# Performance work log

Measured on AMD Instinct MI355X. Metric: run time of the kernel, lower is better.

Reference implementation:

```python
import jax, jax.numpy as jnp
import numpy as np

N_NODES = 50000
N_EDGES = 800000
D_IN = 128
D_OUT = 128


def setup_inputs() -> dict:
    key = jax.random.key(0)
    k1, k2, k3, k4, k5 = jax.random.split(key, 5)
    x = jax.random.normal(k1, (N_NODES, D_IN), dtype=jnp.float32)
    edge_index = jax.random.randint(k2, (2, N_EDGES), 0, N_NODES, dtype=jnp.int64)
    scale = 1.0 / np.sqrt(D_IN)
    W_rel = jax.random.normal(k3, (D_OUT, D_IN), dtype=jnp.float32) * scale
    b_rel = jax.random.normal(k4, (D_OUT,), dtype=jnp.float32) * scale
    W_root = jax.random.normal(k5, (D_OUT, D_IN), dtype=jnp.float32) * scale
    return {"x": x, "edge_index": edge_index, "W_rel": W_rel, "b_rel": b_rel, "W_root": W_root}


def reference(x, edge_index, W_rel, b_rel, W_root):
    # PyG GraphConv (aggr='add'):
    #   out_i = W_rel @ (sum_{j->i} x_j) + b_rel + W_root @ x_i
    # followed by ReLU (normalization=None, dropout=0 -> identity).
    src = edge_index[0]  # message source j
    dst = edge_index[1]  # message target i
    n = x.shape[0]
    agg = jax.ops.segment_sum(x[src], dst, num_segments=n)  # [N, D_IN]
    out = agg @ W_rel.T + b_rel + x @ W_root.T              # [N, D_OUT]
    return jax.nn.relu(out)
```

## Files before the change

### kernel.cpp

```cpp
#include <hip/hip_runtime.h>
#include <hip/hip_bf16.h>


#define N_NODES 50000
#define N_EDGES 800000
#define D 128
#define SLOTS 48
#define NB 3125
#define BCAP 384
#define BINB 196
#define NPB 32
#define KC 32
#define SROW 136

#define CVT_N  (N_NODES * (D / 2))
#define PACK_N (8 * 8 * 64 * 8)

typedef __attribute__((ext_vector_type(8))) short short8;
typedef __attribute__((ext_vector_type(4))) float floatx4;

__device__ __forceinline__ float bf2f(unsigned short u) {
    return __uint_as_float((unsigned int)u << 16);
}
__device__ __forceinline__ unsigned short f2bf(float f) {
    __hip_bfloat16 h = __float2bfloat16(f);
    return *(unsigned short*)&h;
}

__device__ __forceinline__ int wave_detect_i64(const int* __restrict__ ei) {
    int lane = threadIdx.x & 63;
    int v = ei[2 * lane + 1];
    return __ballot(v == 0) == ~0ull;
}

__global__ __launch_bounds__(256) void zero_f4_kernel(float4* __restrict__ p, int n4) {
    int i = blockIdx.x * 256 + threadIdx.x;
    if (i < n4) p[i] = make_float4(0.f, 0.f, 0.f, 0.f);
}

__global__ void detect_kernel(const int* __restrict__ ei, int* __restrict__ flag) {
    if (threadIdx.x == 0 && blockIdx.x == 0) {
        int any = 0;
        for (int i = 0; i < 64; ++i) any |= ei[2 * i + 1];
        flag[0] = (any == 0) ? 1 : 0;
    }
}

__global__ __launch_bounds__(256) void stage1_kernel(const float2* __restrict__ x2,
                                                     ushort2* __restrict__ xb2,
                                                     const float* __restrict__ Wrel,
                                                     const float* __restrict__ Wroot,
                                                     unsigned short* __restrict__ pwc,
                                                     const int* __restrict__ ei,
                                                     int* __restrict__ gcur,
                                                     unsigned* __restrict__ bmem,
                                                     int* __restrict__ ovf_cnt,
                                                     int* __restrict__ ovf) {
    __shared__ int lds_cnt[NB];
    if (blockIdx.x < BINB) {
        int t = threadIdx.x;
        int i64 = wave_detect_i64(ei);
        for (int i = t; i < NB; i += 256) lds_cnt[i] = 0;
        __syncthreads();

        unsigned rec[16];
        int rnk[16];
#pragma unroll
        for (int g = 0; g < 4; ++g) {
            int base = blockIdx.x * 4096 + g * 1024 + t * 4;
            int s0 = -1, s1 = -1, s2 = -1, s3 = -1;
            int d0 = -1, d1 = -1, d2 = -1, d3 = -1;
            if (base < N_EDGES) {
                if (i64) {
                    int4 a = *(const int4*)&ei[2 * base];
                    int4 b = *(const int4*)&ei[2 * base + 4];
                    s0 = a.x; s1 = a.z; s2 = b.x; s3 = b.z;
                    int4 c = *(const int4*)&ei[2 * N_EDGES + 2 * base];
                    int4 e = *(const int4*)&ei[2 * N_EDGES + 2 * base + 4];
                    d0 = c.x; d1 = c.z; d2 = e.x; d3 = e.z;
                } else {
                    int4 sv = *(const int4*)&ei[base];
                    int4 dv = *(const int4*)&ei[N_EDGES + base];
                    s0 = sv.x; s1 = sv.y; s2 = sv.z; s3 = sv.w;
                    d0 = dv.x; d1 = dv.y; d2 = dv.z; d3 = dv.w;
                }
            }
#define BINP(idx, ss, dd)                                                        \
            {                                                                    \
                bool ok = (unsigned)(ss) < N_NODES && (unsigned)(dd) < N_NODES;  \
                rec[idx] = ok ? (((unsigned)(dd) << 16) | (unsigned)(ss))        \
                              : 0xFFFFFFFFu;                                     \
                rnk[idx] = ok ? atomicAdd(&lds_cnt[(unsigned)(dd) >> 4], 1) : 0; \
            }
            BINP(g * 4 + 0, s0, d0)
            BINP(g * 4 + 1, s1, d1)
            BINP(g * 4 + 2, s2, d2)
            BINP(g * 4 + 3, s3, d3)
#undef BINP
        }
        __syncthreads();
        for (int i = t; i < NB; i += 256) {
            int c = lds_cnt[i];
            int b = c ? atomicAdd(&gcur[i], c) : 0;
            lds_cnt[i] = b;
        }
        __syncthreads();
#pragma unroll
        for (int idx = 0; idx < 16; ++idx) {
            unsigned r = rec[idx];
            if (r != 0xFFFFFFFFu) {
                int bk = (int)(r >> 20);
                int pos = lds_cnt[bk] + rnk[idx];
                if (pos < BCAP) {
                    bmem[(size_t)bk * BCAP + pos] = r;
                } else {
                    int o = atomicAdd(ovf_cnt, 1);
                    ovf[2 * o] = (int)(r >> 16);
                    ovf[2 * o + 1] = (int)(r & 0xFFFFu);
                }
            }
        }
    } else {
        int i = (blockIdx.x - BINB) * 256 + threadIdx.x;
        if (i < CVT_N) {
            float2 f = x2[i];
            xb2[i] = make_ushort2(f2bf(f.x), f2bf(f.y));
        } else if (i < CVT_N + PACK_N) {
            int idx  = i - CVT_N;
            int j    = idx & 7;
            int lane = (idx >> 3) & 63;
            int n0   = (idx >> 9) & 7;
            int t    = idx >> 12;
            int n = n0 * 16 + (lane & 15);
            int k = t * 32 + (lane >> 4) * 8 + j;
            float w = (k < D) ? Wrel[n * D + k] : Wroot[n * D + (k - D)];
            pwc[idx] = f2bf(w);
        }
    }
}

__global__ __launch_bounds__(256) void GraphConvLayer_55783035240593_kernel(
        const ushort2* __restrict__ xb2,
        const unsigned short* __restrict__ xb,
        const int* __restrict__ gcur,
        const unsigned* __restrict__ bmem,
        const int* __restrict__ ovf_cnt,
        const int* __restrict__ ovf,
        const unsigned short* __restrict__ pwc,
        const float* __restrict__ b_rel,
        float* __restrict__ out) {
    __shared__ unsigned short sA[16 * SROW];
    __shared__ unsigned short slotsL[16 * SLOTS];
    __shared__ int lc[16];
    int t = threadIdx.x;
    int wid = t >> 6, lane = t & 63;
    int bkt = blockIdx.x;
    int node0 = bkt * 16;

    int n = gcur[bkt];
    int tov = ovf_cnt[0];
    if (t < 16) lc[t] = 0;
    __syncthreads();

    if (n > BCAP) n = BCAP;
    for (int e = t; e < n; e += 256) {
        unsigned r = bmem[(size_t)bkt * BCAP + e];
        int dl = (int)((r >> 16) & 15);
        int p = atomicAdd(&lc[dl], 1);
        if (p < SLOTS) slotsL[dl * SLOTS + p] = (unsigned short)(r & 0xFFFFu);
    }
    __syncthreads();

    for (int pp = 0; pp < 2; ++pp) {
        int la = wid * 4 + pp * 2, lb = la + 1;
        int nodeA = node0 + la, nodeB = node0 + lb;
        int kkA = lc[la], kkB = lc[lb];
        int kA = (kkA > SLOTS) ? 0 : kkA;
        int kB = (kkB > SLOTS) ? 0 : kkB;
        int myA = (lane < kA) ? (int)slotsL[la * SLOTS + lane] : 0;
        int myB = (lane < kB) ? (int)slotsL[lb * SLOTS + lane] : 0;
        float axA = 0.f, ayA = 0.f, axB = 0.f, ayB = 0.f;
        int jmax = kA > kB ? kA : kB;
        for (int j = 0; j < jmax; j += 8) {
            bool doA = j < kA, doB = j < kB;
            ushort2 u[8], v[8];
            if (doA) {
                int s[8];
#pragma unroll
                for (int i = 0; i < 8; ++i) s[i] = __shfl(myA, j + i);
#pragma unroll
                for (int i = 0; i < 8; ++i) u[i] = xb2[(size_t)s[i] * (D / 2) + lane];
            }
            if (doB) {
                int s[8];
#pragma unroll
                for (int i = 0; i < 8; ++i) s[i] = __shfl(myB, j + i);
#pragma unroll
                for (int i = 0; i < 8; ++i) v[i] = xb2[(size_t)s[i] * (D / 2) + lane];
            }
            if (doA) {
#pragma unroll
                for (int i = 0; i < 8; ++i) {
                    float mm = (j + i < kA) ? 1.f : 0.f;
                    axA += mm * bf2f(u[i].x);
                    ayA += mm * bf2f(u[i].y);
                }
            }
            if (doB) {
#pragma unroll
                for (int i = 0; i < 8; ++i) {
                    float mm = (j + i < kB) ? 1.f : 0.f;
                    axB += mm * bf2f(v[i].x);
                    ayB += mm * bf2f(v[i].y);
                }
            }
        }
        if (kkA > SLOTS) {
            for (int e = 0; e < n; ++e) {
                unsigned r = bmem[(size_t)bkt * BCAP + e];
                if ((int)(r >> 16) == nodeA) {
                    ushort2 uu = xb2[(size_t)(r & 0xFFFFu) * (D / 2) + lane];
                    axA += bf2f(uu.x); ayA += bf2f(uu.y);
                }
            }
        }
        if (kkB > SLOTS) {
            for (int e = 0; e < n; ++e) {
                unsigned r = bmem[(size_t)bkt * BCAP + e];
                if ((int)(r >> 16) == nodeB) {
                    ushort2 uu = xb2[(size_t)(r & 0xFFFFu) * (D / 2) + lane];
                    axB += bf2f(uu.x); ayB += bf2f(uu.y);
                }
            }
        }
        if (tov > 0) {
            for (int e2 = 0; e2 < tov; ++e2) {
                int dd = ovf[2 * e2];
                if (dd == nodeA) {
                    ushort2 uu = xb2[(size_t)ovf[2 * e2 + 1] * (D / 2) + lane];
                    axA += bf2f(uu.x); ayA += bf2f(uu.y);
                } else if (dd == nodeB) {
                    ushort2 uu = xb2[(size_t)ovf[2 * e2 + 1] * (D / 2) + lane];
                    axB += bf2f(uu.x); ayB += bf2f(uu.y);
                }
            }
        }
        *(ushort2*)&sA[la * SROW + 2 * lane] = make_ushort2(f2bf(axA), f2bf(ayA));
        *(ushort2*)&sA[lb * SROW + 2 * lane] = make_ushort2(f2bf(axB), f2bf(ayB));
    }
    __syncthreads();

    int m = lane & 15, quad = lane >> 4;
    const unsigned short* arow = &sA[m * SROW + quad * 8];
    const unsigned short* xrow = xb + (size_t)(node0 + m) * D + quad * 8;

    floatx4 acc0 = (floatx4){0.f, 0.f, 0.f, 0.f};
    floatx4 acc1 = (floatx4){0.f, 0.f, 0.f, 0.f};
#pragma unroll
    for (int tt = 0; tt < 8; ++tt) {
        short8 afrag = (tt < 4) ? *(const short8*)(arow + tt * 32)
                                : *(const short8*)(xrow + (tt - 4) * 32);
        const unsigned short* bb = pwc + ((size_t)(tt * 8 + wid * 2) * 64 + lane) * 8;
        short8 b0 = *(const short8*)bb;
        short8 b1 = *(const short8*)(bb + 64 * 8);
        acc0 = __builtin_amdgcn_mfma_f32_16x16x32_bf16(afrag, b0, acc0, 0, 0, 0);
        acc1 = __builtin_amdgcn_mfma_f32_16x16x32_bf16(afrag, b1, acc1, 0, 0, 0);
    }

#pragma unroll
    for (int q = 0; q < 2; ++q) {
        floatx4 a = q ? acc1 : acc0;
        int nn = (wid * 2 + q) * 16 + m;
        float bias = b_rel[nn];
#pragma unroll
        for (int r = 0; r < 4; ++r) {
            int node = node0 + quad * 4 + r;
            out[(size_t)node * D + nn] = fmaxf(a[r] + bias, 0.f);
        }
    }
}

__global__ __launch_bounds__(256) void pack_w_kernel(const float* __restrict__ W,
                                                     float* __restrict__ pw) {
    int idx = blockIdx.x * 256 + threadIdx.x;
    if (idx >= D * D) return;
    int o = idx >> 7, k = idx & 127;
    pw[k * D + o] = W[o * D + k];
}

__global__ __launch_bounds__(256) void hist_kernel(const int* __restrict__ ei,
                                                   int* __restrict__ deg) {
    int i64 = wave_detect_i64(ei);
    int base = (blockIdx.x * 256 + threadIdx.x) * 4;
    if (base >= N_EDGES) return;
    int d0, d1, d2, d3;
    if (i64) {
        int4 a = *(const int4*)&ei[2 * N_EDGES + 2 * base];
        int4 b = *(const int4*)&ei[2 * N_EDGES + 2 * base + 4];
        d0 = a.x; d1 = a.z; d2 = b.x; d3 = b.z;
    } else {
        int4 v = *(const int4*)&ei[N_EDGES + base];
        d0 = v.x; d1 = v.y; d2 = v.z; d3 = v.w;
    }
    if ((unsigned)d0 < N_NODES) atomicAdd(&deg[d0], 1);
    if ((unsigned)d1 < N_NODES) atomicAdd(&deg[d1], 1);
    if ((unsigned)d2 < N_NODES) atomicAdd(&deg[d2], 1);
    if ((unsigned)d3 < N_NODES) atomicAdd(&deg[d3], 1);
}

__device__ __forceinline__ int wave_iscan(int v, int lane) {
#pragma unroll
    for (int off = 1; off < 64; off <<= 1) {
        int u = __shfl_up(v, off, 64);
        if (lane >= off) v += u;
    }
    return v;
}

__global__ __launch_bounds__(1024) void scan_kernel(const int* __restrict__ deg,
                                                    int* __restrict__ offsets,
                                                    int* __restrict__ cursor) {
    __shared__ int wsum[16];
    __shared__ int base_s;
    int t = threadIdx.x, lane = t & 63, w = t >> 6;
    if (t == 0) { base_s = 0; offsets[0] = 0; }
    __syncthreads();
    for (int c0 = 0; c0 < N_NODES; c0 += 1024) {
        int idx = c0 + t;
        int v = (idx < N_NODES) ? deg[idx] : 0;
        int inc = wave_iscan(v, lane);
        if (lane == 63) wsum[w] = inc;
        __syncthreads();
        if (w == 0) {
            int s = (lane < 16) ? wsum[lane] : 0;
            int si = wave_iscan(s, lane);
            if (lane < 16) wsum[lane] = si - s;
        }
        __syncthreads();
        int tot = base_s + wsum[w] + inc;
        if (idx < N_NODES) {
            offsets[idx + 1] = tot;
            cursor[idx] = tot - v;
        }
        __syncthreads();
        if (t == 1023) base_s = tot;
        __syncthreads();
    }
}

__global__ __launch_bounds__(256) void reorder_kernel(const int* __restrict__ ei,
                                                      int* __restrict__ cursor,
                                                      int* __restrict__ csr_src) {
    int i64 = wave_detect_i64(ei);
    int base = (blockIdx.x * 256 + threadIdx.x) * 4;
    if (base >= N_EDGES) return;
    int s0, s1, s2, s3, d0, d1, d2, d3;
    if (i64) {
        int4 a = *(const int4*)&ei[2 * base];
        int4 b = *(const int4*)&ei[2 * base + 4];
        s0 = a.x; s1 = a.z; s2 = b.x; s3 = b.z;
        int4 c = *(const int4*)&ei[2 * N_EDGES + 2 * base];
        int4 e = *(const int4*)&ei[2 * N_EDGES + 2 * base + 4];
        d0 = c.x; d1 = c.z; d2 = e.x; d3 = e.z;
    } else {
        int4 sv = *(const int4*)&ei[base];
        int4 dv = *(const int4*)&ei[N_EDGES + base];
        s0 = sv.x; s1 = sv.y; s2 = sv.z; s3 = sv.w;
        d0 = dv.x; d1 = dv.y; d2 = dv.z; d3 = dv.w;
    }
    bool v0 = (unsigned)s0 < N_NODES && (unsigned)d0 < N_NODES;
    bool v1 = (unsigned)s1 < N_NODES && (unsigned)d1 < N_NODES;
    bool v2 = (unsigned)s2 < N_NODES && (unsigned)d2 < N_NODES;
    bool v3 = (unsigned)s3 < N_NODES && (unsigned)d3 < N_NODES;
    int p0 = v0 ? atomicAdd(&cursor[d0], 1) : 0;
    int p1 = v1 ? atomicAdd(&cursor[d1], 1) : 0;
    int p2 = v2 ? atomicAdd(&cursor[d2], 1) : 0;
    int p3 = v3 ? atomicAdd(&cursor[d3], 1) : 0;
    if (v0) csr_src[p0] = s0;
    if (v1) csr_src[p1] = s1;
    if (v2) csr_src[p2] = s2;
    if (v3) csr_src[p3] = s3;
}

__global__ __launch_bounds__(256) void gather_kernel(const float2* __restrict__ x2,
                                                     const int* __restrict__ csr_src,
                                                     const int* __restrict__ offsets,
                                                     float2* __restrict__ agg2) {
    int node = blockIdx.x * 4 + (threadIdx.x >> 6);
    int lane = threadIdx.x & 63;
    if (node >= N_NODES) return;
    int beg = offsets[node], end = offsets[node + 1];
    float2 acc = make_float2(0.f, 0.f);
    for (int e = beg; e < end; ++e) {
        int s = csr_src[e];
        float2 f = x2[(size_t)s * (D / 2) + lane];
        acc.x += f.x;
        acc.y += f.y;
    }
    agg2[(size_t)node * (D / 2) + lane] = acc;
}

__global__ __launch_bounds__(256) void scatter_kernel(const float2* __restrict__ x2,
                                                      const int* __restrict__ ei,
                                                      const int* __restrict__ flag,
                                                      float* __restrict__ agg) {
    int wave = threadIdx.x >> 6;
    int lane = threadIdx.x & 63;
    int e = blockIdx.x * 4 + wave;
    if (e >= N_EDGES) return;
    int i64 = flag ? flag[0] : 0;
    int s, d;
    if (i64) { s = ei[2 * e]; d = ei[2 * N_EDGES + 2 * e]; }
    else     { s = ei[e];     d = ei[N_EDGES + e]; }
    if ((unsigned)s >= N_NODES || (unsigned)d >= N_NODES) return;
    float2 f = x2[(size_t)s * (D / 2) + lane];
    atomicAdd(&agg[(size_t)d * D + 2 * lane + 0], f.x);
    atomicAdd(&agg[(size_t)d * D + 2 * lane + 1], f.y);
}

__global__ __launch_bounds__(256) void gemm_f32_kernel(
        const float2* __restrict__ x2,
        const float* __restrict__ pwrel,
        const float* __restrict__ pwroot,
        const float* __restrict__ b_rel,
        float* __restrict__ out) {
    __shared__ float sWrel[KC * D];
    __shared__ float sWroot[KC * D];
    __shared__ float2 sAm[NPB * (KC / 2)];
    __shared__ float2 sXm[NPB * (KC / 2)];

    int t = threadIdx.x;
    int node0 = blockIdx.x * NPB;
    int tn = t >> 5;
    int to = t & 31;

    float acc[4][4];
#pragma unroll
    for (int a = 0; a < 4; ++a)
#pragma unroll
        for (int b = 0; b < 4; ++b) acc[a][b] = 0.0f;

    for (int c = 0; c < 4; ++c) {
        __syncthreads();
#pragma unroll
        for (int r = 0; r < 4; ++r) {
            int i = r * 256 + t;
            ((float4*)sWrel)[i]  = ((const float4*)(pwrel  + c * KC * D))[i];
            ((float4*)sWroot)[i] = ((const float4*)(pwroot + c * KC * D))[i];
        }
#pragma unroll
        for (int r = 0; r < 2; ++r) {
            int i = r * 256 + t;
            int n = i >> 4, k2 = i & 15;
            int node = node0 + n;
            float2 av = make_float2(0.f, 0.f), xv = make_float2(0.f, 0.f);
            if (node < N_NODES) {
                av = ((const float2*)out)[(size_t)node * (D / 2) + c * (KC / 2) + k2];
                xv = x2[(size_t)node * (D / 2) + c * (KC / 2) + k2];
            }
            sAm[i] = av;
            sXm[i] = xv;
        }
        __syncthreads();

#pragma unroll
        for (int k2 = 0; k2 < KC / 2; ++k2) {
            float4 wr0 = *(const float4*)&sWrel[(2 * k2 + 0) * D + to * 4];
            float4 wr1 = *(const float4*)&sWrel[(2 * k2 + 1) * D + to * 4];
            float4 wt0 = *(const float4*)&sWroot[(2 * k2 + 0) * D + to * 4];
            float4 wt1 = *(const float4*)&sWroot[(2 * k2 + 1) * D + to * 4];
#pragma unroll
            for (int ni = 0; ni < 4; ++ni) {
                float2 a  = sAm[(tn * 4 + ni) * (KC / 2) + k2];
                float2 xx = sXm[(tn * 4 + ni) * (KC / 2) + k2];
                acc[ni][0] += a.x * wr0.x + a.y * wr1.x + xx.x * wt0.x + xx.y * wt1.x;
                acc[ni][1] += a.x * wr0.y + a.y * wr1.y + xx.x * wt0.y + xx.y * wt1.y;
                acc[ni][2] += a.x * wr0.z + a.y * wr1.z + xx.x * wt0.z + xx.y * wt1.z;
                acc[ni][3] += a.x * wr0.w + a.y * wr1.w + xx.x * wt0.w + xx.y * wt1.w;
            }
        }
    }

    int o0 = to * 4;
    float4 bias = *(const float4*)&b_rel[o0];
#pragma unroll
    for (int ni = 0; ni < 4; ++ni) {
        int node = node0 + tn * 4 + ni;
        if (node >= N_NODES) continue;
        float4 v;
        v.x = fmaxf(acc[ni][0] + bias.x, 0.f);
        v.y = fmaxf(acc[ni][1] + bias.y, 0.f);
        v.z = fmaxf(acc[ni][2] + bias.z, 0.f);
        v.w = fmaxf(acc[ni][3] + bias.w, 0.f);
        *(float4*)&out[(size_t)node * D + o0] = v;
    }
}

__global__ __launch_bounds__(128) void gemm_fallback_kernel(const float* __restrict__ x,
                                                            const float* __restrict__ Wrel,
                                                            const float* __restrict__ Wroot,
                                                            const float* __restrict__ b_rel,
                                                            float* __restrict__ out) {
    __shared__ float rowA[D];
    __shared__ float rowX[D];
    int node = blockIdx.x;
    int o = threadIdx.x;
    rowA[o] = out[(size_t)node * D + o];
    rowX[o] = x[(size_t)node * D + o];
    __syncthreads();
    float acc = b_rel[o];
    const float4* wr = (const float4*)&Wrel[o * D];
    const float4* wt = (const float4*)&Wroot[o * D];
#pragma unroll 8
    for (int k4 = 0; k4 < D / 4; ++k4) {
        float4 w = wr[k4], u = wt[k4];
        const float* a = &rowA[k4 * 4];
        const float* xx = &rowX[k4 * 4];
        acc += a[0] * w.x + a[1] * w.y + a[2] * w.z + a[3] * w.w
             + xx[0] * u.x + xx[1] * u.y + xx[2] * u.z + xx[3] * u.w;
    }
    __syncthreads();
    out[(size_t)node * D + o] = fmaxf(acc, 0.f);
}

extern "C" void kernel_launch(void* const* d_in, const int* in_sizes, int n_in,
                              void* d_out, int out_size, void* d_ws, size_t ws_size,
                              hipStream_t stream) {
    const float* x      = (const float*)d_in[0];
    const int*   ei     = (const int*)d_in[1];
    const float* W_rel  = (const float*)d_in[2];
    const float* b_rel  = (const float*)d_in[3];
    const float* W_root = (const float*)d_in[4];
    float*       out    = (float*)d_out;

    char* p = (char*)d_ws;
    size_t o0 = 16;
    int*            flag    = (int*)p;
    unsigned short* pwc     = (unsigned short*)(p + o0);  o0 += (size_t)PACK_N * 2;
    unsigned short* xb      = (unsigned short*)(p + o0);  o0 += (size_t)N_NODES * D * 2;
    const size_t gcur_pad = ((size_t)NB * 4 + 15) & ~(size_t)15;
    int*            gcur    = (int*)(p + o0);             o0 += gcur_pad;
    int*            ovf_cnt = (int*)(p + o0);             o0 += 16;
    unsigned*       bmem    = (unsigned*)(p + o0);        o0 += (size_t)NB * BCAP * 4;
    int*            ovf     = (int*)(p + o0);             o0 += (size_t)N_EDGES * 8;
    const size_t need_full = o0;

    size_t m0 = 16;
    float* m_pwrel  = (float*)(p + m0);  m0 += (size_t)D * D * 4;
    float* m_pwroot = (float*)(p + m0);  m0 += (size_t)D * D * 4;
    int*   m_deg    = (int*)(p + m0);    m0 += (size_t)N_NODES * 4;
    int*   m_offs   = (int*)(p + m0);    m0 += ((size_t)N_NODES + 1) * 4 + 12;
    m0 &= ~15ull;
    int*   m_csr    = (int*)(p + m0);    m0 += (size_t)N_EDGES * 4;
    const size_t need_mid = m0;
    const size_t need_pw  = 16 + 2 * (size_t)D * D * 4;

    const int eb4 = (N_EDGES / 4 + 255) / 256;

    if (ws_size >= need_full) {
        hipMemsetAsync(gcur, 0, gcur_pad + 16, stream);
        const int prep_total = CVT_N + PACK_N;
        const int grid1 = BINB + (prep_total + 255) / 256;
        stage1_kernel<<<grid1, 256, 0, stream>>>(
            (const float2*)x, (ushort2*)xb, W_rel, W_root, pwc, ei,
            gcur, bmem, ovf_cnt, ovf);
        GraphConvLayer_55783035240593_kernel<<<NB, 256, 0, stream>>>(
            (const ushort2*)xb, xb, gcur, bmem, ovf_cnt, ovf, pwc, b_rel, out);
    } else if (ws_size >= need_mid) {
        pack_w_kernel<<<64, 256, 0, stream>>>(W_rel, m_pwrel);
        pack_w_kernel<<<64, 256, 0, stream>>>(W_root, m_pwroot);
        zero_f4_kernel<<<(N_NODES / 4 + 255) / 256, 256, 0, stream>>>((float4*)m_deg,
                                                                      N_NODES / 4);
        hist_kernel<<<eb4, 256, 0, stream>>>(ei, m_deg);
        scan_kernel<<<1, 1024, 0, stream>>>(m_deg, m_offs, m_deg);
        reorder_kernel<<<eb4, 256, 0, stream>>>(ei, m_deg, m_csr);
        gather_kernel<<<N_NODES / 4, 256, 0, stream>>>((const float2*)x, m_csr,
                                                       m_offs, (float2*)out);
        gemm_f32_kernel<<<(N_NODES + NPB - 1) / NPB, 256, 0, stream>>>(
            (const float2*)x, m_pwrel, m_pwroot, b_rel, out);
    } else {
        bool have_flag = ws_size >= 16;
        bool have_pw   = ws_size >= need_pw;
        if (have_flag) detect_kernel<<<1, 64, 0, stream>>>(ei, flag);
        if (have_pw) {
            pack_w_kernel<<<64, 256, 0, stream>>>(W_rel, m_pwrel);
            pack_w_kernel<<<64, 256, 0, stream>>>(W_root, m_pwroot);
        }
        int n4 = N_NODES * D / 4;
        zero_f4_kernel<<<(n4 + 255) / 256, 256, 0, stream>>>((float4*)out, n4);
        scatter_kernel<<<N_EDGES / 4, 256, 0, stream>>>((const float2*)x, ei,
                                                        have_flag ? flag : nullptr, out);
        if (have_pw)
            gemm_f32_kernel<<<(N_NODES + NPB - 1) / NPB, 256, 0, stream>>>(
                (const float2*)x, m_pwrel, m_pwroot, b_rel, out);
        else
            gemm_fallback_kernel<<<N_NODES, 128, 0, stream>>>(x, W_rel, W_root, b_rel, out);
    }
}
```

Measured before the change: 149.5 us.

## Bin edges by 64-node buckets and gather four nodes per wave with dummy row

```diff
diff --git a/kernel.cpp b/kernel.cpp
--- a/kernel.cpp
+++ b/kernel.cpp
@@ -6,15 +6,18 @@
 #define N_EDGES 800000
 #define D 128
 #define SLOTS 48
-#define NB 3125
-#define BCAP 384
+#define NB 782
+#define TILES 3125
+#define BCAP 1536
 #define BINB 196
 #define NPB 32
 #define KC 32
 #define SROW 136
+#define DUMMY 50000
 
 #define CVT_N  (N_NODES * (D / 2))
 #define PACK_N (8 * 8 * 64 * 8)
+#define ZROW_N (D / 2)
 
 typedef __attribute__((ext_vector_type(8))) short short8;
 typedef __attribute__((ext_vector_type(4))) float floatx4;
@@ -57,6 +60,7 @@
                                                      int* __restrict__ ovf_cnt,
                                                      int* __restrict__ ovf) {
     __shared__ int lds_cnt[NB];
+    __shared__ int lds_base[NB];
     if (blockIdx.x < BINB) {
         int t = threadIdx.x;
         int i64 = wave_detect_i64(ei);
@@ -90,7 +94,7 @@
                 bool ok = (unsigned)(ss) < N_NODES && (unsigned)(dd) < N_NODES;  \
                 rec[idx] = ok ? (((unsigned)(dd) << 16) | (unsigned)(ss))        \
                               : 0xFFFFFFFFu;                                     \
-                rnk[idx] = ok ? atomicAdd(&lds_cnt[(unsigned)(dd) >> 4], 1) : 0; \
+                rnk[idx] = ok ? atomicAdd(&lds_cnt[(unsigned)(dd) >> 6], 1) : 0; \
             }
             BINP(g * 4 + 0, s0, d0)
             BINP(g * 4 + 1, s1, d1)
@@ -101,16 +105,15 @@
         __syncthreads();
         for (int i = t; i < NB; i += 256) {
             int c = lds_cnt[i];
-            int b = c ? atomicAdd(&gcur[i], c) : 0;
-            lds_cnt[i] = b;
+            lds_base[i] = c ? atomicAdd(&gcur[i], c) : 0;
         }
         __syncthreads();
 #pragma unroll
         for (int idx = 0; idx < 16; ++idx) {
             unsigned r = rec[idx];
             if (r != 0xFFFFFFFFu) {
-                int bk = (int)(r >> 20);
-                int pos = lds_cnt[bk] + rnk[idx];
+                int bk = (int)(r >> 22);
+                int pos = lds_base[bk] + rnk[idx];
                 if (pos < BCAP) {
                     bmem[(size_t)bk * BCAP + pos] = r;
                 } else {
@@ -135,11 +138,13 @@
             int k = t * 32 + (lane >> 4) * 8 + j;
             float w = (k < D) ? Wrel[n * D + k] : Wroot[n * D + (k - D)];
             pwc[idx] = f2bf(w);
-        }
-    }
-}
-
-__global__ __launch_bounds__(256) void GraphConvLayer_55783035240593_kernel(
+        } else if (i < CVT_N + PACK_N + ZROW_N) {
+            xb2[CVT_N + (i - CVT_N - PACK_N)] = make_ushort2(0, 0);
+        }
+    }
+}
+
+__global__ __launch_bounds__(256, 8) void GraphConvLayer_55783035240593_kernel(
         const ushort2* __restrict__ xb2,
         const unsigned short* __restrict__ xb,
         const int* __restrict__ gcur,
@@ -154,100 +159,114 @@
     __shared__ int lc[16];
     int t = threadIdx.x;
     int wid = t >> 6, lane = t & 63;
-    int bkt = blockIdx.x;
-    int node0 = bkt * 16;
+    int tile = blockIdx.x;
+    int bkt = tile >> 2;
+    unsigned q = (unsigned)(tile & 3);
+    int node0 = tile * 16;
 
     int n = gcur[bkt];
     int tov = ovf_cnt[0];
     if (t < 16) lc[t] = 0;
+    for (int i = t; i < 16 * SLOTS / 2; i += 256)
+        ((unsigned*)slotsL)[i] = (DUMMY << 16) | DUMMY;
     __syncthreads();
 
     if (n > BCAP) n = BCAP;
     for (int e = t; e < n; e += 256) {
         unsigned r = bmem[(size_t)bkt * BCAP + e];
+        if (((r >> 20) & 3u) != q) continue;
         int dl = (int)((r >> 16) & 15);
         int p = atomicAdd(&lc[dl], 1);
         if (p < SLOTS) slotsL[dl * SLOTS + p] = (unsigned short)(r & 0xFFFFu);
     }
     __syncthreads();
 
-    for (int pp = 0; pp < 2; ++pp) {
-        int la = wid * 4 + pp * 2, lb = la + 1;
-        int nodeA = node0 + la, nodeB = node0 + lb;
-        int kkA = lc[la], kkB = lc[lb];
-        int kA = (kkA > SLOTS) ? 0 : kkA;
-        int kB = (kkB > SLOTS) ? 0 : kkB;
-        int myA = (lane < kA) ? (int)slotsL[la * SLOTS + lane] : 0;
-        int myB = (lane < kB) ? (int)slotsL[lb * SLOTS + lane] : 0;
-        float axA = 0.f, ayA = 0.f, axB = 0.f, ayB = 0.f;
-        int jmax = kA > kB ? kA : kB;
-        for (int j = 0; j < jmax; j += 8) {
-            bool doA = j < kA, doB = j < kB;
-            ushort2 u[8], v[8];
-            if (doA) {
-                int s[8];
-#pragma unroll
-                for (int i = 0; i < 8; ++i) s[i] = __shfl(myA, j + i);
-#pragma unroll
-                for (int i = 0; i < 8; ++i) u[i] = xb2[(size_t)s[i] * (D / 2) + lane];
+    int kk0 = lc[wid * 4 + 0], kk1 = lc[wid * 4 + 1];
+    int kk2 = lc[wid * 4 + 2], kk3 = lc[wid * 4 + 3];
+    int kc0 = (kk0 > SLOTS) ? 0 : kk0;
+    int kc1 = (kk1 > SLOTS) ? 0 : kk1;
+    int kc2 = (kk2 > SLOTS) ? 0 : kk2;
+    int kc3 = (kk3 > SLOTS) ? 0 : kk3;
+    int sl = lane < SLOTS ? lane : 0;
+    int my0 = (kk0 > SLOTS) ? DUMMY : (int)slotsL[(wid * 4 + 0) * SLOTS + sl];
+    int my1 = (kk1 > SLOTS) ? DUMMY : (int)slotsL[(wid * 4 + 1) * SLOTS + sl];
+    int my2 = (kk2 > SLOTS) ? DUMMY : (int)slotsL[(wid * 4 + 2) * SLOTS + sl];
+    int my3 = (kk3 > SLOTS) ? DUMMY : (int)slotsL[(wid * 4 + 3) * SLOTS + sl];
+    int jmax = kc0 > kc1 ? kc0 : kc1;
+    jmax = kc2 > jmax ? kc2 : jmax;
+    jmax = kc3 > jmax ? kc3 : jmax;
+    float ax0 = 0.f, ay0 = 0.f, ax1 = 0.f, ay1 = 0.f;
+    float ax2 = 0.f, ay2 = 0.f, ax3 = 0.f, ay3 = 0.f;
+    for (int j = 0; j < jmax; j += 8) {
+        ushort2 u0[8], u1[8], u2[8], u3[8];
+#pragma unroll
+        for (int v = 0; v < 8; ++v) {
+            int s = __shfl(my0, j + v);
+            u0[v] = xb2[(size_t)s * (D / 2) + lane];
+        }
+#pragma unroll
+        for (int v = 0; v < 8; ++v) {
+            int s = __shfl(my1, j + v);
+            u1[v] = xb2[(size_t)s * (D / 2) + lane];
+        }
+#pragma unroll
+        for (int v = 0; v < 8; ++v) {
+            int s = __shfl(my2, j + v);
+            u2[v] = xb2[(size_t)s * (D / 2) + lane];
+        }
+#pragma unroll
+        for (int v = 0; v < 8; ++v) {
+            int s = __shfl(my3, j + v);
+            u3[v] = xb2[(size_t)s * (D / 2) + lane];
+        }
+#pragma unroll
+        for (int v = 0; v < 8; ++v) { ax0 += bf2f(u0[v].x); ay0 += bf2f(u0[v].y); }
+#pragma unroll
+        for (int v = 0; v < 8; ++v) { ax1 += bf2f(u1[v].x); ay1 += bf2f(u1[v].y); }
+#pragma unroll
+        for (int v = 0; v < 8; ++v) { ax2 += bf2f(u2[v].x); ay2 += bf2f(u2[v].y); }
+#pragma unroll
+        for (int v = 0; v < 8; ++v) { ax3 += bf2f(u3[v].x); ay3 += bf2f(u3[v].y); }
+    }
+
+    int nodeb = node0 + wid * 4;
+    if (kk0 > SLOTS || kk1 > SLOTS || kk2 > SLOTS || kk3 > SLOTS) {
+        for (int e = 0; e < n; ++e) {
+            unsigned r = bmem[(size_t)bkt * BCAP + e];
+            int dd = (int)(r >> 16);
+            ushort2 uu;
+            if (kk0 > SLOTS && dd == nodeb + 0) {
+                uu = xb2[(size_t)(r & 0xFFFFu) * (D / 2) + lane];
+                ax0 += bf2f(uu.x); ay0 += bf2f(uu.y);
+            } else if (kk1 > SLOTS && dd == nodeb + 1) {
+                uu = xb2[(size_t)(r & 0xFFFFu) * (D / 2) + lane];
+                ax1 += bf2f(uu.x); ay1 += bf2f(uu.y);
+            } else if (kk2 > SLOTS && dd == nodeb + 2) {
+                uu = xb2[(size_t)(r & 0xFFFFu) * (D / 2) + lane];
+                ax2 += bf2f(uu.x); ay2 += bf2f(uu.y);
+            } else if (kk3 > SLOTS && dd == nodeb + 3) {
+                uu = xb2[(size_t)(r & 0xFFFFu) * (D / 2) + lane];
+                ax3 += bf2f(uu.x); ay3 += bf2f(uu.y);
             }
-            if (doB) {
-                int s[8];
-#pragma unroll
-                for (int i = 0; i < 8; ++i) s[i] = __shfl(myB, j + i);
-#pragma unroll
-                for (int i = 0; i < 8; ++i) v[i] = xb2[(size_t)s[i] * (D / 2) + lane];
+        }
+    }
+    if (tov > 0) {
+        for (int e2 = 0; e2 < tov; ++e2) {
+            int dd = ovf[2 * e2];
+            int rel = dd - nodeb;
+            if ((unsigned)rel < 4u) {
+                ushort2 uu = xb2[(size_t)ovf[2 * e2 + 1] * (D / 2) + lane];
+                if (rel == 0)      { ax0 += bf2f(uu.x); ay0 += bf2f(uu.y); }
+                else if (rel == 1) { ax1 += bf2f(uu.x); ay1 += bf2f(uu.y); }
+                else if (rel == 2) { ax2 += bf2f(uu.x); ay2 += bf2f(uu.y); }
+                else               { ax3 += bf2f(uu.x); ay3 += bf2f(uu.y); }
             }
-            if (doA) {
-#pragma unroll
-                for (int i = 0; i < 8; ++i) {
-                    float mm = (j + i < kA) ? 1.f : 0.f;
-                    axA += mm * bf2f(u[i].x);
-                    ayA += mm * bf2f(u[i].y);
-                }
-            }
-            if (doB) {
-#pragma unroll
-                for (int i = 0; i < 8; ++i) {
-                    float mm = (j + i < kB) ? 1.f : 0.f;
-                    axB += mm * bf2f(v[i].x);
-                    ayB += mm * bf2f(v[i].y);
-                }
-            }
-        }
-        if (kkA > SLOTS) {
-            for (int e = 0; e < n; ++e) {
-                unsigned r = bmem[(size_t)bkt * BCAP + e];
-                if ((int)(r >> 16) == nodeA) {
-                    ushort2 uu = xb2[(size_t)(r & 0xFFFFu) * (D / 2) + lane];
-                    axA += bf2f(uu.x); ayA += bf2f(uu.y);
-                }
-            }
-        }
-        if (kkB > SLOTS) {
-            for (int e = 0; e < n; ++e) {
-                unsigned r = bmem[(size_t)bkt * BCAP + e];
-                if ((int)(r >> 16) == nodeB) {
-                    ushort2 uu = xb2[(size_t)(r & 0xFFFFu) * (D / 2) + lane];
-                    axB += bf2f(uu.x); ayB += bf2f(uu.y);
-                }
-            }
-        }
-        if (tov > 0) {
-            for (int e2 = 0; e2 < tov; ++e2) {
-                int dd = ovf[2 * e2];
-                if (dd == nodeA) {
-                    ushort2 uu = xb2[(size_t)ovf[2 * e2 + 1] * (D / 2) + lane];
-                    axA += bf2f(uu.x); ayA += bf2f(uu.y);
-                } else if (dd == nodeB) {
-                    ushort2 uu = xb2[(size_t)ovf[2 * e2 + 1] * (D / 2) + lane];
-                    axB += bf2f(uu.x); ayB += bf2f(uu.y);
-                }
-            }
-        }
-        *(ushort2*)&sA[la * SROW + 2 * lane] = make_ushort2(f2bf(axA), f2bf(ayA));
-        *(ushort2*)&sA[lb * SROW + 2 * lane] = make_ushort2(f2bf(axB), f2bf(ayB));
-    }
+        }
+    }
+    *(ushort2*)&sA[(wid * 4 + 0) * SROW + 2 * lane] = make_ushort2(f2bf(ax0), f2bf(ay0));
+    *(ushort2*)&sA[(wid * 4 + 1) * SROW + 2 * lane] = make_ushort2(f2bf(ax1), f2bf(ay1));
+    *(ushort2*)&sA[(wid * 4 + 2) * SROW + 2 * lane] = make_ushort2(f2bf(ax2), f2bf(ay2));
+    *(ushort2*)&sA[(wid * 4 + 3) * SROW + 2 * lane] = make_ushort2(f2bf(ax3), f2bf(ay3));
     __syncthreads();
 
     int m = lane & 15, quad = lane >> 4;
@@ -268,9 +287,9 @@
     }
 
 #pragma unroll
-    for (int q = 0; q < 2; ++q) {
-        floatx4 a = q ? acc1 : acc0;
-        int nn = (wid * 2 + q) * 16 + m;
+    for (int qq = 0; qq < 2; ++qq) {
+        floatx4 a = qq ? acc1 : acc0;
+        int nn = (wid * 2 + qq) * 16 + m;
         float bias = b_rel[nn];
 #pragma unroll
         for (int r = 0; r < 4; ++r) {
@@ -537,7 +556,7 @@
     size_t o0 = 16;
     int*            flag    = (int*)p;
     unsigned short* pwc     = (unsigned short*)(p + o0);  o0 += (size_t)PACK_N * 2;
-    unsigned short* xb      = (unsigned short*)(p + o0);  o0 += (size_t)N_NODES * D * 2;
+    unsigned short* xb      = (unsigned short*)(p + o0);  o0 += (size_t)(N_NODES + 1) * D * 2;
     const size_t gcur_pad = ((size_t)NB * 4 + 15) & ~(size_t)15;
     int*            gcur    = (int*)(p + o0);             o0 += gcur_pad;
     int*            ovf_cnt = (int*)(p + o0);             o0 += 16;
@@ -559,12 +578,12 @@
 
     if (ws_size >= need_full) {
         hipMemsetAsync(gcur, 0, gcur_pad + 16, stream);
-        const int prep_total = CVT_N + PACK_N;
+        const int prep_total = CVT_N + PACK_N + ZROW_N;
         const int grid1 = BINB + (prep_total + 255) / 256;
         stage1_kernel<<<grid1, 256, 0, stream>>>(
             (const float2*)x, (ushort2*)xb, W_rel, W_root, pwc, ei,
             gcur, bmem, ovf_cnt, ovf);
-        GraphConvLayer_55783035240593_kernel<<<NB, 256, 0, stream>>>(
+        GraphConvLayer_55783035240593_kernel<<<TILES, 256, 0, stream>>>(
             (const ushort2*)xb, xb, gcur, bmem, ovf_cnt, ovf, pwc, b_rel, out);
     } else if (ws_size >= need_mid) {
         pack_w_kernel<<<64, 256, 0, stream>>>(W_rel, m_pwrel);
```

Result: no change. 147.8 us (-1.1%).
